# Performance work log

Measured on AMD Instinct MI355X. Metric: run time of the kernel, lower is better.

Reference implementation:

```python
import jax, jax.numpy as jnp
import numpy as np

WS = 7        # window_size
SHIFT = 3     # shift_size
NH = 12       # num_heads
HD = 32       # head_dim
C = 384       # dim
HH = 56       # height
WW = 56       # width
EPS = 1e-5


def _rel_pos_index():
    coords = np.stack(np.meshgrid(np.arange(WS), np.arange(WS), indexing='ij')).reshape(2, -1)
    rel = (coords[:, :, None] - coords[:, None, :]).transpose(1, 2, 0)
    rel[:, :, 0] += WS - 1
    rel[:, :, 1] += WS - 1
    rel[:, :, 0] *= 2 * WS - 1
    return rel.sum(-1)  # (49, 49) int


def _attn_mask():
    # shift mask, computed statically (shift_size > 0 path)
    img = np.zeros((HH, WW))
    slices = (slice(0, -WS), slice(-WS, -SHIFT), slice(-SHIFT, None))
    cnt = 0
    for hs in slices:
        for ws in slices:
            img[hs, ws] = cnt
            cnt += 1
    mw = img.reshape(HH // WS, WS, WW // WS, WS).transpose(0, 2, 1, 3).reshape(-1, WS * WS)
    diff = mw[:, None, :] - mw[:, :, None]  # (nW, 49, 49)
    return np.where(diff != 0, -100.0, 0.0).astype(np.float32)


_REL_IDX = jnp.asarray(_rel_pos_index())
_MASK = jnp.asarray(_attn_mask())


def _layernorm(x, g, b):
    mu = jnp.mean(x, axis=-1, keepdims=True)
    var = jnp.mean(jnp.square(x - mu), axis=-1, keepdims=True)
    return (x - mu) * jax.lax.rsqrt(var + EPS) * g + b


def setup_inputs() -> dict:
    key = jax.random.key(0)
    ks = jax.random.split(key, 10)
    s = 0.02
    return {
        'hidden_states': jax.random.normal(ks[0], (32, HH * WW, C), jnp.float32),
        'ln1_g': jnp.ones((C,), jnp.float32),
        'ln1_b': jnp.zeros((C,), jnp.float32),
        'qkv_w': jax.random.normal(ks[1], (3 * C, C), jnp.float32) * s,
        'qkv_b': jnp.zeros((3 * C,), jnp.float32),
        'out_w': jax.random.normal(ks[2], (C, C), jnp.float32) * s,
        'out_b': jnp.zeros((C,), jnp.float32),
        'rel_bias_table': jax.random.normal(ks[3], ((2 * WS - 1) ** 2, NH), jnp.float32) * s,
        'ln2_g': jnp.ones((C,), jnp.float32),
        'ln2_b': jnp.zeros((C,), jnp.float32),
        'fc1_w': jax.random.normal(ks[4], (4 * C, C), jnp.float32) * s,
        'fc1_b': jnp.zeros((4 * C,), jnp.float32),
        'fc2_w': jax.random.normal(ks[5], (C, 4 * C), jnp.float32) * s,
        'fc2_b': jnp.zeros((C,), jnp.float32),
        'height': HH,
        'width': WW,
    }


def reference(hidden_states, ln1_g, ln1_b, qkv_w, qkv_b, out_w, out_b,
              rel_bias_table, ln2_g, ln2_b, fc1_w, fc1_b, fc2_w, fc2_b,
              height, width):
    B = hidden_states.shape[0]
    nWh, nWw = HH // WS, WW // WS
    nW = nWh * nWw
    L = WS * WS

    shortcut = hidden_states
    x = _layernorm(hidden_states, ln1_g, ln1_b).reshape(B, HH, WW, C)
    x = jnp.roll(x, (-SHIFT, -SHIFT), axis=(1, 2))
    # window partition -> (B*nW, 49, C)
    xw = x.reshape(B, nWh, WS, nWw, WS, C).transpose(0, 1, 3, 2, 4, 5).reshape(B * nW, L, C)

    qkv = xw @ qkv_w.T + qkv_b
    q, k, v = jnp.split(qkv, 3, axis=-1)
    q = q.reshape(-1, L, NH, HD).transpose(0, 2, 1, 3)  # (N, h, 49, d)
    k = k.reshape(-1, L, NH, HD).transpose(0, 2, 1, 3)
    v = v.reshape(-1, L, NH, HD).transpose(0, 2, 1, 3)

    scale = HD ** -0.5
    attn = jnp.einsum('nhqd,nhkd->nhqk', q, k) * scale
    bias = rel_bias_table[_REL_IDX.reshape(-1)].reshape(L, L, NH).transpose(2, 0, 1)  # (h, 49, 49)
    attn = attn + bias[None]
    attn = attn.reshape(B, nW, NH, L, L) + _MASK[None, :, None]
    attn = jax.nn.softmax(attn, axis=-1).reshape(B * nW, NH, L, L)

    out = jnp.einsum('nhqk,nhkd->nhqd', attn, v).transpose(0, 2, 1, 3).reshape(B * nW, L, C)
    out = out @ out_w.T + out_b

    # window reverse + un-shift
    out = out.reshape(B, nWh, nWw, WS, WS, C).transpose(0, 1, 3, 2, 4, 5).reshape(B, HH, WW, C)
    out = jnp.roll(out, (SHIFT, SHIFT), axis=(1, 2)).reshape(B, HH * WW, C)

    x = shortcut + out  # drop_path is identity (rate 0 / eval)
    h2 = _layernorm(x, ln2_g, ln2_b)
    mlp = jax.nn.gelu(h2 @ fc1_w.T + fc1_b, approximate=False) @ fc2_w.T + fc2_b
    return x + mlp
```

## Files before the change

### kernel.cpp

```cpp
#include <hip/hip_runtime.h>
#include <cstdint>
#include <cstddef>

using u16 = unsigned short;
using u32 = unsigned int;

typedef __attribute__((ext_vector_type(8))) short bf16x8;
typedef __attribute__((ext_vector_type(4))) float f32x4;

__device__ __forceinline__ u16 f2bf(float f) {
  union { float f; u32 u; } v; v.f = f;
  u32 r = v.u + 0x7FFFu + ((v.u >> 16) & 1u);
  return (u16)(r >> 16);
}
__device__ __forceinline__ float bf2f(u16 h) {
  union { u32 u; float f; } v; v.u = ((u32)h) << 16;
  return v.f;
}

__device__ __forceinline__ void gl_lds16(const void* g, void* l) {
  __builtin_amdgcn_global_load_lds(
      (const __attribute__((address_space(1))) void*)g,
      (__attribute__((address_space(3))) void*)l, 16, 0, 0);
}

__device__ __forceinline__ float gelu_fast(float v) {
  float u = v * (0.7978845608f + 0.0356774081f * v * v);
  float e = __expf(-2.f * fabsf(u));
  float th = (1.f - e) / (1.f + e);
  th = (u >= 0.f) ? th : -th;
  return 0.5f * v * (1.f + th);
}

__global__ __launch_bounds__(256) void k_f2bf4(
    const float* __restrict__ a0, const float* __restrict__ a1,
    const float* __restrict__ a2, const float* __restrict__ a3,
    u16* __restrict__ d0, u16* __restrict__ d1, u16* __restrict__ d2,
    u16* __restrict__ d3) {
  int i = blockIdx.x * 256 + threadIdx.x;
  if (i < 442368) d0[i] = f2bf(a0[i]);
  else if (i < 589824) d1[i - 442368] = f2bf(a1[i - 442368]);
  else if (i < 1179648) d2[i - 589824] = f2bf(a2[i - 589824]);
  else if (i < 1769472) d3[i - 1179648] = f2bf(a3[i - 1179648]);
}

__global__ __launch_bounds__(256) void k_tbl(const float* __restrict__ relt,
                                             float* __restrict__ tbl) {
  int id = blockIdx.x * 256 + threadIdx.x;
  if (id >= 196608) return;
  int qi = id & 3, c = (id >> 2) & 15, g = (id >> 6) & 3;
  int r = (id >> 8) & 3, kj = (id >> 10) & 3;
  int wt = (id >> 12) & 3, h = id >> 14;
  int i = qi * 16 + c;
  int j = kj * 16 + g * 4 + r;
  float v;
  if (j >= 49) {
    v = -3e38f;
  } else {
    int ii = i < 49 ? i : 48;
    int r1 = ii / 7, c1 = ii % 7, r2 = j / 7, c2 = j % 7;
    v = relt[((r1 - r2 + 6) * 13 + (c1 - c2 + 6)) * 12 + h];
    int rr1 = (wt & 2) ? (r1 < 4 ? 1 : 2) : 0;
    int rr2 = (wt & 2) ? (r2 < 4 ? 1 : 2) : 0;
    int cc1 = (wt & 1) ? (c1 < 4 ? 1 : 2) : 0;
    int cc2 = (wt & 1) ? (c2 < 4 ? 1 : 2) : 0;
    if (rr1 != rr2 || cc1 != cc2) v -= 100.f;
  }
  tbl[id] = v;
}

template <int GATHER>
__global__ __launch_bounds__(256) void k_ln(const float* __restrict__ x,
                                            const float* __restrict__ g,
                                            const float* __restrict__ b,
                                            u16* __restrict__ out) {
  int wave = threadIdx.x >> 6, lane = threadIdx.x & 63;
  int idx = blockIdx.x * 4 + wave;
  int src;
  if (GATHER) {
    int n = idx / 49, l = idx % 49;
    int bb = n >> 6, wi = n & 63;
    int wh = wi >> 3, ww = wi & 7;
    int r = l / 7, c = l % 7;
    int sr = wh * 7 + r + 3; if (sr >= 56) sr -= 56;
    int sc = ww * 7 + c + 3; if (sc >= 56) sc -= 56;
    src = bb * 3136 + sr * 56 + sc;
  } else {
    src = idx;
  }
  const float* xi = x + (size_t)src * 384;
  float2 v[3];
  float s = 0.f, sq = 0.f;
#pragma unroll
  for (int p = 0; p < 3; ++p) {
    v[p] = *(const float2*)(xi + p * 128 + lane * 2);
    s += v[p].x + v[p].y;
    sq += v[p].x * v[p].x + v[p].y * v[p].y;
  }
#pragma unroll
  for (int o = 32; o; o >>= 1) {
    s += __shfl_xor(s, o);
    sq += __shfl_xor(sq, o);
  }
  float mu = s * (1.f / 384.f);
  float var = sq * (1.f / 384.f) - mu * mu;
  float rstd = rsqrtf(var + 1e-5f);
  u16* oo = out + (size_t)idx * 384;
#pragma unroll
  for (int p = 0; p < 3; ++p) {
    int e = p * 128 + lane * 2;
    u16 o0 = f2bf((v[p].x - mu) * rstd * g[e] + b[e]);
    u16 o1 = f2bf((v[p].y - mu) * rstd * g[e + 1] + b[e + 1]);
    u32 pk = (u32)o0 | ((u32)o1 << 16);
    *(u32*)(oo + e) = pk;
  }
}

enum { EPI_QKV = 0, EPI_PROJ = 1, EPI_GELU = 2, EPI_FC2 = 3 };

template <int EPI>
__global__ __launch_bounds__(512, 2) void k_gemm3(
    const u16* __restrict__ A, const u16* __restrict__ Bw,
    const float* __restrict__ bias, u16* __restrict__ obf,
    float* __restrict__ of32, const float* __restrict__ addsrc,
    int K, int lda, int ldb, int ldc, int NT) {
  __shared__ u16 As[256 * 64];
  __shared__ u16 Bs[128 * 64];
  const int nwg = gridDim.x;
  const int q = nwg >> 3, r = nwg & 7;
  const int xcd = blockIdx.x & 7, rank = blockIdx.x >> 3;
  const int swz = (xcd < r ? xcd * (q + 1) : r * (q + 1) + (xcd - r) * q) + rank;
  const int m0 = (swz / NT) * 256, n0 = (swz % NT) * 128;

  const int tid = threadIdx.x;
  const int wid = tid >> 6, lane = tid & 63;
  const int wr = wid >> 1, wc = wid & 1;

  const int srow = tid >> 3;
  const int scol = 8 * ((tid & 7) ^ (srow & 7));
  const size_t abase = (size_t)(m0 + srow) * lda + scol;
  const size_t bbase = (size_t)(n0 + srow) * ldb + scol;
  const int dbase = wid * 512;

  f32x4 acc[4][4] = {};
  const int lrow = lane & 15;
  const int g8 = (lane >> 4) * 8;
  const int rx = (lrow & 7) << 3;

  const int NTK = K >> 6;

  for (int t = 0; t < NTK; ++t) {
    const int k0 = t << 6;
#pragma unroll
    for (int i = 0; i < 4; ++i)
      gl_lds16(A + abase + (size_t)(i * 64) * lda + k0,
               As + i * 4096 + dbase);
#pragma unroll
    for (int i = 0; i < 2; ++i)
      gl_lds16(Bw + bbase + (size_t)(i * 64) * ldb + k0,
               Bs + i * 4096 + dbase);
    __syncthreads();
    __builtin_amdgcn_s_setprio(1);
#pragma unroll
    for (int kk = 0; kk < 64; kk += 32) {
      bf16x8 af[4], bf[4];
#pragma unroll
      for (int mi = 0; mi < 4; ++mi) {
        int row = wr * 64 + mi * 16 + lrow;
        af[mi] = *(const bf16x8*)(&As[row * 64 + ((kk + g8) ^ rx)]);
      }
#pragma unroll
      for (int ni = 0; ni < 4; ++ni) {
        int row = wc * 64 + ni * 16 + lrow;
        bf[ni] = *(const bf16x8*)(&Bs[row * 64 + ((kk + g8) ^ rx)]);
      }
#pragma unroll
      for (int mi = 0; mi < 4; ++mi)
#pragma unroll
        for (int ni = 0; ni < 4; ++ni)
          acc[mi][ni] = __builtin_amdgcn_mfma_f32_16x16x32_bf16(
              af[mi], bf[ni], acc[mi][ni], 0, 0, 0);
    }
    __builtin_amdgcn_s_setprio(0);
    __syncthreads();
  }

  const int erow = (lane >> 4) * 4;
  const int ecol = lane & 15;
#pragma unroll
  for (int mi = 0; mi < 4; ++mi) {
#pragma unroll
    for (int ni = 0; ni < 4; ++ni) {
      int gcol = n0 + wc * 64 + ni * 16 + ecol;
      float bv = bias[gcol];
#pragma unroll
      for (int r4 = 0; r4 < 4; ++r4) {
        int grow = m0 + wr * 64 + mi * 16 + erow + r4;
        float v = acc[mi][ni][r4] + bv;
        if (EPI == EPI_QKV) {
          float vv = (gcol < 384) ? v * 0.17677669529663689f : v;
          obf[(size_t)grow * ldc + gcol] = f2bf(vv);
        } else if (EPI == EPI_GELU) {
          obf[(size_t)grow * ldc + gcol] = f2bf(gelu_fast(v));
        } else if (EPI == EPI_PROJ) {
          int nwin = grow / 49, l = grow % 49;
          int bb = nwin >> 6, wi = nwin & 63;
          int wh = wi >> 3, ww = wi & 7;
          int rr = l / 7, cc = l % 7;
          int sr = wh * 7 + rr + 3; if (sr >= 56) sr -= 56;
          int sc = ww * 7 + cc + 3; if (sc >= 56) sc -= 56;
          size_t idx = ((size_t)(bb * 3136 + sr * 56 + sc)) * 384 + gcol;
          of32[idx] = addsrc[idx] + v;
        } else {
          size_t idx = (size_t)grow * 384 + gcol;
          of32[idx] = of32[idx] + v;
        }
      }
    }
  }
}

__global__ __launch_bounds__(64) void k_attn2(const u16* __restrict__ qkv,
                                              const float* __restrict__ tbl,
                                              u16* __restrict__ out) {
  __shared__ u16 P[64 * 64];
  const int bx = blockIdx.x;
  const int n = bx / 12, h = bx - n * 12;
  const int lane = threadIdx.x & 63;
  const int g = lane >> 4, c = lane & 15;
  const u16* base = qkv + (size_t)n * 56448 + h * 32;
  const int wi = n & 63;
  const int wt = (((wi >> 3) == 7) ? 2 : 0) | (((wi & 7) == 7) ? 1 : 0);
  const float* T = tbl + (size_t)((h << 2) | wt) * 4096;

  f32x4 st[4][4];
#pragma unroll
  for (int kj = 0; kj < 4; ++kj)
#pragma unroll
    for (int r = 0; r < 4; ++r) {
      f32x4 v4 = *(const f32x4*)(T + ((((kj * 4 + r) * 4 + g) * 16 + c) << 2));
#pragma unroll
      for (int qi = 0; qi < 4; ++qi) st[kj][qi][r] = v4[qi];
    }

  bf16x8 qf[4], kf[4];
#pragma unroll
  for (int t = 0; t < 4; ++t) {
    int row = t * 16 + c; if (row > 48) row = 48;
    qf[t] = *(const bf16x8*)(base + (size_t)row * 1152 + g * 8);
    kf[t] = *(const bf16x8*)(base + (size_t)row * 1152 + 384 + g * 8);
  }

  __builtin_amdgcn_s_setprio(1);
#pragma unroll
  for (int kj = 0; kj < 4; ++kj)
#pragma unroll
    for (int qi = 0; qi < 4; ++qi)
      st[kj][qi] = __builtin_amdgcn_mfma_f32_16x16x32_bf16(kf[kj], qf[qi],
                                                           st[kj][qi], 0, 0, 0);
  __builtin_amdgcn_s_setprio(0);

#pragma unroll
  for (int qi = 0; qi < 4; ++qi) {
    float m = -3e38f;
#pragma unroll
    for (int kj = 0; kj < 4; ++kj)
#pragma unroll
      for (int r = 0; r < 4; ++r) m = fmaxf(m, st[kj][qi][r]);
    m = fmaxf(m, __shfl_xor(m, 16));
    m = fmaxf(m, __shfl_xor(m, 32));
    float sum = 0.f;
#pragma unroll
    for (int kj = 0; kj < 4; ++kj)
#pragma unroll
      for (int r = 0; r < 4; ++r) {
        float e = __expf(st[kj][qi][r] - m);
        st[kj][qi][r] = e;
        sum += e;
      }
    sum += __shfl_xor(sum, 16);
    sum += __shfl_xor(sum, 32);
    float inv = 1.f / sum;
    int i = qi * 16 + c;
#pragma unroll
    for (int kj = 0; kj < 4; ++kj)
#pragma unroll
      for (int hh = 0; hh < 2; ++hh) {
        u32 pk = (u32)f2bf(st[kj][qi][2 * hh] * inv) |
                 ((u32)f2bf(st[kj][qi][2 * hh + 1] * inv) << 16);
        int idx = (i * 64 + kj * 16 + g * 4 + 2 * hh) ^ ((i & 7) << 3);
        *(u32*)(P + idx) = pk;
      }
  }

  f32x4 o[4][2] = {};
#pragma unroll
  for (int k0 = 0; k0 < 2; ++k0) {
    bf16x8 pa[4], vb[2];
#pragma unroll
    for (int qi = 0; qi < 4; ++qi) {
      int qq = qi * 16 + c;
      pa[qi] = *(const bf16x8*)(P + ((qq * 64 + k0 * 32 + g * 8) ^ ((qq & 7) << 3)));
    }
#pragma unroll
    for (int ni = 0; ni < 2; ++ni) {
      union { bf16x8 v; u16 a[8]; } vu;
#pragma unroll
      for (int e = 0; e < 8; ++e) {
        int j = k0 * 32 + g * 8 + e;
        int jr = j > 48 ? 48 : j;
        vu.a[e] = base[(size_t)jr * 1152 + 768 + ni * 16 + c];
      }
      vb[ni] = vu.v;
    }
    __builtin_amdgcn_s_setprio(1);
#pragma unroll
    for (int ni = 0; ni < 2; ++ni)
#pragma unroll
      for (int qi = 0; qi < 4; ++qi)
        o[qi][ni] = __builtin_amdgcn_mfma_f32_16x16x32_bf16(pa[qi], vb[ni],
                                                            o[qi][ni], 0, 0, 0);
    __builtin_amdgcn_s_setprio(0);
  }

  u16* ob = out + (size_t)n * 18816 + h * 32;
#pragma unroll
  for (int qi = 0; qi < 4; ++qi)
#pragma unroll
    for (int r = 0; r < 4; ++r) {
      int qq = qi * 16 + g * 4 + r;
      if (qq < 49) {
#pragma unroll
        for (int ni = 0; ni < 2; ++ni)
          ob[(size_t)qq * 384 + ni * 16 + c] = f2bf(o[qi][ni][r]);
      }
    }
}

extern "C" void kernel_launch(void* const* d_in, const int* in_sizes, int n_in,
                              void* d_out, int out_size, void* d_ws,
                              size_t ws_size, hipStream_t stream) {
  const float* hidden = (const float*)d_in[0];
  const float* ln1g = (const float*)d_in[1];
  const float* ln1b = (const float*)d_in[2];
  const float* qkvw = (const float*)d_in[3];
  const float* qkvb = (const float*)d_in[4];
  const float* outw = (const float*)d_in[5];
  const float* outb = (const float*)d_in[6];
  const float* relt = (const float*)d_in[7];
  const float* ln2g = (const float*)d_in[8];
  const float* ln2b = (const float*)d_in[9];
  const float* fc1w = (const float*)d_in[10];
  const float* fc1b = (const float*)d_in[11];
  const float* fc2w = (const float*)d_in[12];
  const float* fc2b = (const float*)d_in[13];
  float* out = (float*)d_out;

  u16* wq = (u16*)d_ws;
  u16* wo = wq + 442368;
  u16* w1 = wo + 147456;
  u16* w2 = w1 + 589824;
  u16* xw = w2 + 589824;
  u16* qkv = xw + 38535168;
  u16* xn = qkv;
  u16* hbuf = xn + 38535168;
  float* tbl = (float*)wq;

  k_f2bf4<<<6912, 256, 0, stream>>>(qkvw, outw, fc1w, fc2w, wq, wo, w1, w2);

  k_ln<1><<<25088, 256, 0, stream>>>(hidden, ln1g, ln1b, xw);

  k_gemm3<EPI_QKV><<<392 * 9, 512, 0, stream>>>(
      xw, wq, qkvb, qkv, nullptr, nullptr, 384, 384, 384, 1152, 9);

  k_tbl<<<768, 256, 0, stream>>>(relt, tbl);

  k_attn2<<<24576, 64, 0, stream>>>(qkv, tbl, xw);

  k_gemm3<EPI_PROJ><<<392 * 3, 512, 0, stream>>>(
      xw, wo, outb, nullptr, out, hidden, 384, 384, 384, 384, 3);

  k_ln<0><<<25088, 256, 0, stream>>>(out, ln2g, ln2b, xn);

  for (int ch = 0; ch < 2; ++ch) {
    const u16* xa = xn + (size_t)ch * 50176 * 384;
    float* oc = out + (size_t)ch * 50176 * 384;
    k_gemm3<EPI_GELU><<<196 * 12, 512, 0, stream>>>(
        xa, w1, fc1b, hbuf, nullptr, nullptr, 384, 384, 384, 1536, 12);
    k_gemm3<EPI_FC2><<<196 * 3, 512, 0, stream>>>(
        hbuf, w2, fc2b, nullptr, oc, nullptr, 1536, 1536, 1536, 384, 3);
  }
}
```

Baseline: 905.3 us.

## Store attention residual as bf16 and pack four attention heads per block

The projection epilogue now writes the residual sum x as bf16 into a scratch buffer instead of fp32 into the output. A new bf16-input layernorm reads that buffer, and the FC2 epilogue reads the bf16 residual instead of re-reading fp32 output. This cuts fp32 traffic in the residual path at the cost of rounding the residual stream to bf16, which loses precision. Separately, the attention kernel now runs four waves per 256-thread block, each with its own LDS tile, to cut the number of tiny blocks.

```diff
diff --git a/kernel.cpp b/kernel.cpp
--- a/kernel.cpp
+++ b/kernel.cpp
@@ -116,6 +116,43 @@
   }
 }
 
+__global__ __launch_bounds__(256) void k_ln_bf(const u16* __restrict__ x,
+                                               const float* __restrict__ g,
+                                               const float* __restrict__ b,
+                                               u16* __restrict__ out) {
+  int wave = threadIdx.x >> 6, lane = threadIdx.x & 63;
+  int idx = blockIdx.x * 4 + wave;
+  const u16* xi = x + (size_t)idx * 384;
+  float v[6];
+  float s = 0.f, sq = 0.f;
+#pragma unroll
+  for (int p = 0; p < 3; ++p) {
+    u32 pk = *(const u32*)(xi + p * 128 + lane * 2);
+    float a = bf2f((u16)(pk & 0xffff));
+    float c2 = bf2f((u16)(pk >> 16));
+    v[2 * p] = a; v[2 * p + 1] = c2;
+    s += a + c2;
+    sq += a * a + c2 * c2;
+  }
+#pragma unroll
+  for (int o = 32; o; o >>= 1) {
+    s += __shfl_xor(s, o);
+    sq += __shfl_xor(sq, o);
+  }
+  float mu = s * (1.f / 384.f);
+  float var = sq * (1.f / 384.f) - mu * mu;
+  float rstd = rsqrtf(var + 1e-5f);
+  u16* oo = out + (size_t)idx * 384;
+#pragma unroll
+  for (int p = 0; p < 3; ++p) {
+    int e = p * 128 + lane * 2;
+    u16 o0 = f2bf((v[2 * p] - mu) * rstd * g[e] + b[e]);
+    u16 o1 = f2bf((v[2 * p + 1] - mu) * rstd * g[e + 1] + b[e + 1]);
+    u32 pk = (u32)o0 | ((u32)o1 << 16);
+    *(u32*)(oo + e) = pk;
+  }
+}
+
 enum { EPI_QKV = 0, EPI_PROJ = 1, EPI_GELU = 2, EPI_FC2 = 3 };
 
 template <int EPI>
@@ -123,7 +160,7 @@
     const u16* __restrict__ A, const u16* __restrict__ Bw,
     const float* __restrict__ bias, u16* __restrict__ obf,
     float* __restrict__ of32, const float* __restrict__ addsrc,
-    int K, int lda, int ldb, int ldc, int NT) {
+    const u16* __restrict__ xres, int K, int lda, int ldb, int ldc, int NT) {
   __shared__ u16 As[256 * 64];
   __shared__ u16 Bs[128 * 64];
   const int nwg = gridDim.x;
@@ -210,24 +247,26 @@
           int sr = wh * 7 + rr + 3; if (sr >= 56) sr -= 56;
           int sc = ww * 7 + cc + 3; if (sc >= 56) sc -= 56;
           size_t idx = ((size_t)(bb * 3136 + sr * 56 + sc)) * 384 + gcol;
-          of32[idx] = addsrc[idx] + v;
+          obf[idx] = f2bf(addsrc[idx] + v);
         } else {
           size_t idx = (size_t)grow * 384 + gcol;
-          of32[idx] = of32[idx] + v;
+          of32[idx] = bf2f(xres[idx]) + v;
         }
       }
     }
   }
 }
 
-__global__ __launch_bounds__(64) void k_attn2(const u16* __restrict__ qkv,
-                                              const float* __restrict__ tbl,
-                                              u16* __restrict__ out) {
-  __shared__ u16 P[64 * 64];
-  const int bx = blockIdx.x;
-  const int n = bx / 12, h = bx - n * 12;
+__global__ __launch_bounds__(256) void k_attn2(const u16* __restrict__ qkv,
+                                               const float* __restrict__ tbl,
+                                               u16* __restrict__ out) {
+  __shared__ u16 P[4][64 * 64];
+  const int wid = threadIdx.x >> 6;
+  const int id = blockIdx.x * 4 + wid;
+  const int n = id / 12, h = id - n * 12;
   const int lane = threadIdx.x & 63;
   const int g = lane >> 4, c = lane & 15;
+  u16* Pw = P[wid];
   const u16* base = qkv + (size_t)n * 56448 + h * 32;
   const int wi = n & 63;
   const int wt = (((wi >> 3) == 7) ? 2 : 0) | (((wi & 7) == 7) ? 1 : 0);
@@ -289,7 +328,7 @@
         u32 pk = (u32)f2bf(st[kj][qi][2 * hh] * inv) |
                  ((u32)f2bf(st[kj][qi][2 * hh + 1] * inv) << 16);
         int idx = (i * 64 + kj * 16 + g * 4 + 2 * hh) ^ ((i & 7) << 3);
-        *(u32*)(P + idx) = pk;
+        *(u32*)(Pw + idx) = pk;
       }
   }
 
@@ -300,7 +339,8 @@
 #pragma unroll
     for (int qi = 0; qi < 4; ++qi) {
       int qq = qi * 16 + c;
-      pa[qi] = *(const bf16x8*)(P + ((qq * 64 + k0 * 32 + g * 8) ^ ((qq & 7) << 3)));
+      pa[qi] =
+          *(const bf16x8*)(Pw + ((qq * 64 + k0 * 32 + g * 8) ^ ((qq & 7) << 3)));
     }
 #pragma unroll
     for (int ni = 0; ni < 2; ++ni) {
@@ -362,8 +402,9 @@
   u16* w2 = w1 + 589824;
   u16* xw = w2 + 589824;
   u16* qkv = xw + 38535168;
-  u16* xn = qkv;
-  u16* hbuf = xn + 38535168;
+  u16* xbuf = qkv;
+  u16* hbuf = qkv + 38535168;
+  u16* xn = xw;
   float* tbl = (float*)wq;
 
   k_f2bf4<<<6912, 256, 0, stream>>>(qkvw, outw, fc1w, fc2w, wq, wo, w1, w2);
@@ -371,23 +412,24 @@
   k_ln<1><<<25088, 256, 0, stream>>>(hidden, ln1g, ln1b, xw);
 
   k_gemm3<EPI_QKV><<<392 * 9, 512, 0, stream>>>(
-      xw, wq, qkvb, qkv, nullptr, nullptr, 384, 384, 384, 1152, 9);
+      xw, wq, qkvb, qkv, nullptr, nullptr, nullptr, 384, 384, 384, 1152, 9);
 
   k_tbl<<<768, 256, 0, stream>>>(relt, tbl);
 
-  k_attn2<<<24576, 64, 0, stream>>>(qkv, tbl, xw);
+  k_attn2<<<6144, 256, 0, stream>>>(qkv, tbl, xw);
 
   k_gemm3<EPI_PROJ><<<392 * 3, 512, 0, stream>>>(
-      xw, wo, outb, nullptr, out, hidden, 384, 384, 384, 384, 3);
-
-  k_ln<0><<<25088, 256, 0, stream>>>(out, ln2g, ln2b, xn);
+      xw, wo, outb, xbuf, nullptr, hidden, nullptr, 384, 384, 384, 384, 3);
+
+  k_ln_bf<<<25088, 256, 0, stream>>>(xbuf, ln2g, ln2b, xn);
 
   for (int ch = 0; ch < 2; ++ch) {
     const u16* xa = xn + (size_t)ch * 50176 * 384;
+    const u16* xr = xbuf + (size_t)ch * 50176 * 384;
     float* oc = out + (size_t)ch * 50176 * 384;
     k_gemm3<EPI_GELU><<<196 * 12, 512, 0, stream>>>(
-        xa, w1, fc1b, hbuf, nullptr, nullptr, 384, 384, 384, 1536, 12);
+        xa, w1, fc1b, hbuf, nullptr, nullptr, nullptr, 384, 384, 384, 1536, 12);
     k_gemm3<EPI_FC2><<<196 * 3, 512, 0, stream>>>(
-        hbuf, w2, fc2b, nullptr, oc, nullptr, 1536, 1536, 1536, 384, 3);
-  }
-}
+        hbuf, w2, fc2b, nullptr, oc, nullptr, xr, 1536, 1536, 1536, 384, 3);
+  }
+}
```

Result: faster. 858.3 us (-5.2%).
